# Optimization experiments

Hardware: AMD Instinct MI355X
Metric: run time of the kernel (lower is better)

## Reference

```python
import jax, jax.numpy as jnp
import numpy as np

N_NODES = 50000
N_EDGES = 800000
HIDDEN = 128


def setup_inputs() -> dict:
    key = jax.random.key(0)
    k_emb, k_ei, k1, k2, k3, kb1, kb2, kb3 = jax.random.split(key, 8)
    emb = jax.random.normal(k_emb, (N_NODES, HIDDEN), dtype=jnp.float32)
    edge_index = jax.random.randint(k_ei, (2, N_EDGES), 0, N_NODES, dtype=jnp.int64)
    h = HIDDEN
    # MLP([2h, 4h, h, 1]) weights, Kaiming-uniform-ish init
    def lin(k, fan_in, fan_out):
        bound = 1.0 / np.sqrt(fan_in)
        return jax.random.uniform(k, (fan_in, fan_out), jnp.float32, -bound, bound)
    W1 = lin(k1, 2 * h, 4 * h)
    b1 = jax.random.uniform(kb1, (4 * h,), jnp.float32, -1.0 / np.sqrt(2 * h), 1.0 / np.sqrt(2 * h))
    W2 = lin(k2, 4 * h, h)
    b2 = jax.random.uniform(kb2, (h,), jnp.float32, -1.0 / np.sqrt(4 * h), 1.0 / np.sqrt(4 * h))
    W3 = lin(k3, h, 1)
    b3 = jax.random.uniform(kb3, (1,), jnp.float32, -1.0 / np.sqrt(h), 1.0 / np.sqrt(h))
    return {"emb": emb, "edge_index": edge_index,
            "W1": W1, "b1": b1, "W2": W2, "b2": b2, "W3": W3, "b3": b3}


def reference(emb, edge_index, W1, b1, W2, b2, W3, b3):
    # learn_edge_att=True path: gather endpoints, concat, 3-layer MLP
    col, row = edge_index[0], edge_index[1]
    f12 = jnp.concatenate([emb[col], emb[row]], axis=-1)  # [E, 2h]
    x = jax.nn.relu(f12 @ W1 + b1)                         # [E, 4h]
    x = jax.nn.relu(x @ W2 + b2)                           # [E, h]
    att_log_logits = x @ W3 + b3                           # [E, 1]
    return att_log_logits
```

## Files before the change

### kernel.cpp

```cpp
#include <hip/hip_runtime.h>
#include <hip/hip_bf16.h>
#include <stdint.h>

#define N_EDGES   800000
#define N_NODESC  50000
#define HID       128

typedef __attribute__((ext_vector_type(8))) short bf16x8;
typedef __attribute__((ext_vector_type(4))) float f32x4;
typedef __attribute__((ext_vector_type(4))) unsigned int u32x4;

__device__ __forceinline__ short f2bf(float f) {
    union { float f; uint32_t u; } v; v.f = f;
    uint32_t r = v.u + 0x7FFFu + ((v.u >> 16) & 1u);
    return (short)(r >> 16);
}

__device__ __forceinline__ uint32_t packbf2(float lo, float hi) {
    float2 t; t.x = lo; t.y = hi;
    __hip_bfloat162 h = __float22bfloat162_rn(t);
    uint32_t u;
    __builtin_memcpy(&u, &h, 4);
    return u;
}

__device__ __forceinline__ uint32_t addrelu2(uint32_t a, uint32_t b) {
    __hip_bfloat162 ha, hb;
    __builtin_memcpy(&ha, &a, 4);
    __builtin_memcpy(&hb, &b, 4);
    __hip_bfloat162 s = __hadd2(ha, hb);
    uint32_t x;
    __builtin_memcpy(&x, &s, 4);
    uint32_t neg = (x & 0x80008000u) >> 15;
    return x & ~(neg * 0xFFFFu);
}
__device__ __forceinline__ bf16x8 addrelu8(u32x4 p, u32x4 q) {
    u32x4 r;
    #pragma unroll
    for (int j = 0; j < 4; ++j) r[j] = addrelu2(p[j], q[j]);
    bf16x8 out;
    __builtin_memcpy(&out, &r, 16);
    return out;
}

#define PQ_OFF    0UL
#define W1S_OFF   102400000UL
#define W2S_OFF   (W1S_OFF + 262144UL)
#define CNT_OFF   (W2S_OFF + 131072UL)
#define BSUM_OFF  (CNT_OFF + 1605632UL)
#define SPK_OFF   (BSUM_OFF + 8192UL)
#define POS_OFF   (SPK_OFF + 3200000UL)
#define TMP_OFF   (POS_OFF + 3200000UL)

#define NBINS     50176
#define NSEG      8
#define SCAN_N    (NSEG * NBINS)
#define SCANA_BLOCKS 1568

__global__ __launch_bounds__(256) void swizzle_kernel(const float* __restrict__ W1,
                                                      const float* __restrict__ W2,
                                                      short* __restrict__ W1s,
                                                      short* __restrict__ W2s) {
    int t = blockIdx.x * 256 + threadIdx.x;
    int lane = t & 63;
    int kq = lane >> 4;
    int nn = lane & 15;
    if (t < 16384) {
        int frag = t >> 6;
        int kc = frag >> 6;
        int nt = frag & 63;
        int n = nt * 16 + nn;
        int kbase = kc * 32 + kq * 8;
        bf16x8 v;
        #pragma unroll
        for (int j = 0; j < 8; ++j) {
            int k = kbase + j;
            float f = (n < 512) ? W1[k * 512 + n] : W1[(128 + k) * 512 + (n - 512)];
            v[j] = f2bf(f);
        }
        *(bf16x8*)(W1s + frag * 512 + lane * 8) = v;
    } else if (t < 24576) {
        int t2 = t - 16384;
        int frag = t2 >> 6;
        int kc = frag >> 3;
        int nt = frag & 7;
        int n = nt * 16 + nn;
        int kbase = kc * 32 + kq * 8;
        bf16x8 v;
        #pragma unroll
        for (int j = 0; j < 8; ++j) v[j] = f2bf(W2[(kbase + j) * HID + n]);
        *(bf16x8*)(W2s + frag * 512 + lane * 8) = v;
    }
}

__global__ __launch_bounds__(256) void precompute_kernel(const float* __restrict__ emb,
                                                         const short* __restrict__ W1s,
                                                         const float* __restrict__ b1,
                                                         short* __restrict__ PQ) {
    __shared__ short tile[4][16][272];
    int lane = threadIdx.x & 63;
    int w = threadIdx.x >> 6;
    int nb = blockIdx.x * 16;
    int m = lane & 15;
    int kq = lane >> 4;

    const float* arow = emb + (size_t)(nb + m) * 128 + kq * 8;

    f32x4 acc[16];
    #pragma unroll
    for (int i = 0; i < 16; ++i) acc[i] = (f32x4){0.f, 0.f, 0.f, 0.f};

    #pragma unroll
    for (int kc = 0; kc < 4; ++kc) {
        f32x4 x0 = *(const f32x4*)(arow + kc * 32);
        f32x4 x1 = *(const f32x4*)(arow + kc * 32 + 4);
        u32x4 au;
        au[0] = packbf2(x0[0], x0[1]); au[1] = packbf2(x0[2], x0[3]);
        au[2] = packbf2(x1[0], x1[1]); au[3] = packbf2(x1[2], x1[3]);
        bf16x8 a;
        __builtin_memcpy(&a, &au, 16);
        #pragma unroll
        for (int nt = 0; nt < 16; ++nt) {
            int frag = kc * 64 + (w * 16 + nt);
            bf16x8 b = *(const bf16x8*)(W1s + frag * 512 + lane * 8);
            acc[nt] = __builtin_amdgcn_mfma_f32_16x16x32_bf16(a, b, acc[nt], 0, 0, 0);
        }
    }

    #pragma unroll
    for (int nt = 0; nt < 16; ++nt) {
        int n = w * 256 + nt * 16 + m;
        float bias = (n < 512) ? b1[n] : 0.0f;
        #pragma unroll
        for (int r = 0; r < 4; ++r)
            tile[w][kq * 4 + r][nt * 16 + m] = f2bf(acc[nt][r] + bias);
    }

    #pragma unroll
    for (int s = 0; s < 8; ++s) {
        int row = s * 2 + (lane >> 5);
        int chunk = lane & 31;
        bf16x8 v = *(const bf16x8*)(&tile[w][row][chunk * 8]);
        *(bf16x8*)(PQ + (size_t)(nb + row) * 1024 + w * 256 + chunk * 8) = v;
    }
}


__global__ __launch_bounds__(256) void hist_kernel(const int* __restrict__ ei,
                                                   int* __restrict__ counts) {
    int e = blockIdx.x * 256 + threadIdx.x;
    int seg = blockIdx.x & 7;
    atomicAdd(&counts[seg * NBINS + ei[e]], 1);
}

__global__ __launch_bounds__(256) void scanA_kernel(int* __restrict__ counts,
                                                    int* __restrict__ bsum) {
    __shared__ int sm[256];
    int t = threadIdx.x;
    int e = blockIdx.x * 256 + t;
    int addr = (e & 7) * NBINS + (e >> 3);
    int v = counts[addr];
    sm[t] = v;
    __syncthreads();
    #pragma unroll
    for (int off = 1; off < 256; off <<= 1) {
        int y = (t >= off) ? sm[t - off] : 0;
        __syncthreads();
        sm[t] += y;
        __syncthreads();
    }
    counts[addr] = sm[t] - v;
    if (t == 255) bsum[blockIdx.x] = sm[t];
}

__global__ __launch_bounds__(256) void finalizeC_kernel(int* __restrict__ counts,
                                                        const int* __restrict__ bsum) {
    __shared__ int wsum[4];
    int t = threadIdx.x;
    int b = blockIdx.x;
    int v = 0;
    for (int idx = t; idx < b; idx += 256) v += bsum[idx];
    #pragma unroll
    for (int off = 1; off < 64; off <<= 1) v += __shfl_xor(v, off, 64);
    if ((t & 63) == 0) wsum[t >> 6] = v;
    __syncthreads();
    int base = wsum[0] + wsum[1] + wsum[2] + wsum[3];
    int e = b * 256 + t;
    counts[(e & 7) * NBINS + (e >> 3)] += base;
}

__global__ __launch_bounds__(256) void scatter_kernel(const int* __restrict__ ei,
                                                      int* __restrict__ cursor,
                                                      unsigned int* __restrict__ spk,
                                                      int* __restrict__ pos) {
    int e = blockIdx.x * 256 + threadIdx.x;
    int seg = blockIdx.x & 7;
    int c = ei[e];
    int r = ei[N_EDGES + e];
    int p = atomicAdd(&cursor[seg * NBINS + c], 1);
    spk[p] = ((unsigned int)r << 16) | (unsigned int)c;
    pos[e] = p;
}

__global__ __launch_bounds__(256, 3) void edge_kernel(const short* __restrict__ PQ,
                                                      const unsigned int* __restrict__ spk,
                                                      const short* __restrict__ W2s,
                                                      const float* __restrict__ b2,
                                                      const float* __restrict__ W3,
                                                      const float* __restrict__ b3,
                                                      float* __restrict__ tmp) {
    int lane = threadIdx.x & 63;
    int w = threadIdx.x >> 6;
    int e0 = blockIdx.x * 128 + w * 32;
    int m = lane & 15;
    int kq = lane >> 4;

    unsigned int pk = spk[e0 + (lane & 31)];

    const short* pb[2];
    const short* qb[2];
    #pragma unroll
    for (int t = 0; t < 2; ++t) {
        unsigned int v = __shfl(pk, t * 16 + m, 64);
        int ce = (int)(v & 0xFFFFu);
        int re = (int)(v >> 16);
        pb[t] = PQ + (size_t)ce * 1024 + kq * 8;
        qb[t] = PQ + (size_t)re * 1024 + 512 + kq * 8;
    }

    f32x4 acc[2][8];
    #pragma unroll
    for (int t = 0; t < 2; ++t)
        #pragma unroll
        for (int nt = 0; nt < 8; ++nt) acc[t][nt] = (f32x4){0.f, 0.f, 0.f, 0.f};

    #pragma unroll
    for (int kc = 0; kc < 16; ++kc) {
        u32x4 p[2], q[2];
        #pragma unroll
        for (int t = 0; t < 2; ++t) {
            p[t] = *(const u32x4*)(pb[t] + kc * 32);
            q[t] = *(const u32x4*)(qb[t] + kc * 32);
        }
        bf16x8 b[8];
        #pragma unroll
        for (int nt = 0; nt < 8; ++nt)
            b[nt] = *(const bf16x8*)(W2s + (kc * 8 + nt) * 512 + lane * 8);
        #pragma unroll
        for (int t = 0; t < 2; ++t) {
            bf16x8 a = addrelu8(p[t], q[t]);
            #pragma unroll
            for (int nt = 0; nt < 8; ++nt)
                acc[t][nt] = __builtin_amdgcn_mfma_f32_16x16x32_bf16(a, b[nt], acc[t][nt], 0, 0, 0);
        }
    }

    float b2v[8], w3v[8];
    #pragma unroll
    for (int nt = 0; nt < 8; ++nt) {
        b2v[nt] = b2[nt * 16 + m];
        w3v[nt] = W3[nt * 16 + m];
    }
    float b3s = b3[0];
    #pragma unroll
    for (int t = 0; t < 2; ++t) {
        float partial[4] = {0.f, 0.f, 0.f, 0.f};
        #pragma unroll
        for (int nt = 0; nt < 8; ++nt) {
            #pragma unroll
            for (int r = 0; r < 4; ++r) {
                float x2 = acc[t][nt][r] + b2v[nt];
                x2 = x2 > 0.f ? x2 : 0.f;
                partial[r] += x2 * w3v[nt];
            }
        }
        #pragma unroll
        for (int r = 0; r < 4; ++r) {
            #pragma unroll
            for (int off = 1; off < 16; off <<= 1)
                partial[r] += __shfl_xor(partial[r], off, 64);
        }
        if (m == 0) {
            f32x4 v;
            #pragma unroll
            for (int r = 0; r < 4; ++r) v[r] = partial[r] + b3s;
            *(f32x4*)(tmp + e0 + t * 16 + kq * 4) = v;
        }
    }
}

__global__ __launch_bounds__(256) void permute_kernel(const float* __restrict__ tmp,
                                                      const int* __restrict__ pos,
                                                      float* __restrict__ out) {
    int e = blockIdx.x * 256 + threadIdx.x;
    out[e] = tmp[pos[e]];
}

extern "C" void kernel_launch(void* const* d_in, const int* in_sizes, int n_in,
                              void* d_out, int out_size, void* d_ws, size_t ws_size,
                              hipStream_t stream) {
    const float* emb = (const float*)d_in[0];
    const int*   ei  = (const int*)d_in[1];
    const float* W1  = (const float*)d_in[2];
    const float* b1  = (const float*)d_in[3];
    const float* W2  = (const float*)d_in[4];
    const float* b2  = (const float*)d_in[5];
    const float* W3  = (const float*)d_in[6];
    const float* b3  = (const float*)d_in[7];
    float* out = (float*)d_out;

    short* PQ   = (short*)((char*)d_ws + PQ_OFF);
    short* W1s  = (short*)((char*)d_ws + W1S_OFF);
    short* W2s  = (short*)((char*)d_ws + W2S_OFF);
    int* counts = (int*)((char*)d_ws + CNT_OFF);
    int* bsum   = (int*)((char*)d_ws + BSUM_OFF);
    unsigned int* spk = (unsigned int*)((char*)d_ws + SPK_OFF);
    int* pos    = (int*)((char*)d_ws + POS_OFF);
    float* tmp  = (float*)((char*)d_ws + TMP_OFF);

    swizzle_kernel<<<96, 256, 0, stream>>>(W1, W2, W1s, W2s);
    hipMemsetAsync(counts, 0, SCAN_N * sizeof(int), stream);
    hist_kernel<<<N_EDGES / 256, 256, 0, stream>>>(ei, counts);
    scanA_kernel<<<SCANA_BLOCKS, 256, 0, stream>>>(counts, bsum);
    finalizeC_kernel<<<SCANA_BLOCKS, 256, 0, stream>>>(counts, bsum);
    scatter_kernel<<<N_EDGES / 256, 256, 0, stream>>>(ei, counts, spk, pos);

    precompute_kernel<<<N_NODESC / 16, 256, 0, stream>>>(emb, W1s, b1, PQ);
    edge_kernel<<<N_EDGES / 128, 256, 0, stream>>>(PQ, spk, W2s, b2, W3, b3, tmp);
    permute_kernel<<<N_EDGES / 256, 256, 0, stream>>>(tmp, pos, out);
}
```

Measured before the change: 452.9 us.

## Replace global-atomic counting sort with coarse-bin per-block LDS histogram sort

Swaps the exact per-node counting sort (global atomics over 8 segmented copies of 50k bins) for a coarse 16-node-bin sort built from per-block LDS histograms over 128 blocks, followed by the same scan and a per-block LDS cursor scatter. This removes the memset and the global atomic traffic in the histogram and scatter phases. Edges end up only partially sorted (grouped by col>>4), which may weaken gather locality in edge_kernel. Using only 128 blocks for the histogram and scatter may also underfill the GPU.

```diff
diff --git a/kernel.cpp b/kernel.cpp
--- a/kernel.cpp
+++ b/kernel.cpp
@@ -52,10 +52,11 @@
 #define POS_OFF   (SPK_OFF + 3200000UL)
 #define TMP_OFF   (POS_OFF + 3200000UL)
 
-#define NBINS     50176
-#define NSEG      8
-#define SCAN_N    (NSEG * NBINS)
-#define SCANA_BLOCKS 1568
+#define NBIN2     3136
+#define NBLK2     128
+#define EPB       (N_EDGES / NBLK2)
+#define SCAN_N    (NBIN2 * NBLK2)
+#define SCAN_BLOCKS 1568
 
 __global__ __launch_bounds__(256) void swizzle_kernel(const float* __restrict__ W1,
                                                       const float* __restrict__ W2,
@@ -146,20 +147,27 @@
 }
 
 
-__global__ __launch_bounds__(256) void hist_kernel(const int* __restrict__ ei,
-                                                   int* __restrict__ counts) {
-    int e = blockIdx.x * 256 + threadIdx.x;
-    int seg = blockIdx.x & 7;
-    atomicAdd(&counts[seg * NBINS + ei[e]], 1);
-}
-
-__global__ __launch_bounds__(256) void scanA_kernel(int* __restrict__ counts,
+__global__ __launch_bounds__(256) void binhist_kernel(const int* __restrict__ ei,
+                                                      int* __restrict__ cnt) {
+    __shared__ int h[NBIN2];
+    int t = threadIdx.x;
+    int b = blockIdx.x;
+    for (int i = t; i < NBIN2; i += 256) h[i] = 0;
+    __syncthreads();
+    int base = b * EPB;
+    for (int i = t; i < EPB; i += 256)
+        atomicAdd(&h[ei[base + i] >> 4], 1);
+    __syncthreads();
+    for (int i = t; i < NBIN2; i += 256) cnt[b * NBIN2 + i] = h[i];
+}
+
+__global__ __launch_bounds__(256) void scanA_kernel(int* __restrict__ cnt,
                                                     int* __restrict__ bsum) {
     __shared__ int sm[256];
     int t = threadIdx.x;
-    int e = blockIdx.x * 256 + t;
-    int addr = (e & 7) * NBINS + (e >> 3);
-    int v = counts[addr];
+    int L = blockIdx.x * 256 + t;
+    int addr = (L & (NBLK2 - 1)) * NBIN2 + (L >> 7);
+    int v = cnt[addr];
     sm[t] = v;
     __syncthreads();
     #pragma unroll
@@ -169,11 +177,11 @@
         sm[t] += y;
         __syncthreads();
     }
-    counts[addr] = sm[t] - v;
+    cnt[addr] = sm[t] - v;
     if (t == 255) bsum[blockIdx.x] = sm[t];
 }
 
-__global__ __launch_bounds__(256) void finalizeC_kernel(int* __restrict__ counts,
+__global__ __launch_bounds__(256) void finalizeC_kernel(int* __restrict__ cnt,
                                                         const int* __restrict__ bsum) {
     __shared__ int wsum[4];
     int t = threadIdx.x;
@@ -185,21 +193,28 @@
     if ((t & 63) == 0) wsum[t >> 6] = v;
     __syncthreads();
     int base = wsum[0] + wsum[1] + wsum[2] + wsum[3];
-    int e = b * 256 + t;
-    counts[(e & 7) * NBINS + (e >> 3)] += base;
-}
-
-__global__ __launch_bounds__(256) void scatter_kernel(const int* __restrict__ ei,
-                                                      int* __restrict__ cursor,
-                                                      unsigned int* __restrict__ spk,
-                                                      int* __restrict__ pos) {
-    int e = blockIdx.x * 256 + threadIdx.x;
-    int seg = blockIdx.x & 7;
-    int c = ei[e];
-    int r = ei[N_EDGES + e];
-    int p = atomicAdd(&cursor[seg * NBINS + c], 1);
-    spk[p] = ((unsigned int)r << 16) | (unsigned int)c;
-    pos[e] = p;
+    int L = b * 256 + t;
+    cnt[(L & (NBLK2 - 1)) * NBIN2 + (L >> 7)] += base;
+}
+
+__global__ __launch_bounds__(256) void binscatter_kernel(const int* __restrict__ ei,
+                                                         const int* __restrict__ cnt,
+                                                         unsigned int* __restrict__ spk,
+                                                         int* __restrict__ pos) {
+    __shared__ int cur[NBIN2];
+    int t = threadIdx.x;
+    int b = blockIdx.x;
+    for (int i = t; i < NBIN2; i += 256) cur[i] = cnt[b * NBIN2 + i];
+    __syncthreads();
+    int base = b * EPB;
+    for (int i = t; i < EPB; i += 256) {
+        int e = base + i;
+        int c = ei[e];
+        int r = ei[N_EDGES + e];
+        int p = atomicAdd(&cur[c >> 4], 1);
+        spk[p] = ((unsigned int)r << 16) | (unsigned int)c;
+        pos[e] = p;
+    }
 }
 
 __global__ __launch_bounds__(256, 3) void edge_kernel(const short* __restrict__ PQ,
@@ -312,18 +327,17 @@
     short* PQ   = (short*)((char*)d_ws + PQ_OFF);
     short* W1s  = (short*)((char*)d_ws + W1S_OFF);
     short* W2s  = (short*)((char*)d_ws + W2S_OFF);
-    int* counts = (int*)((char*)d_ws + CNT_OFF);
+    int* cnt    = (int*)((char*)d_ws + CNT_OFF);
     int* bsum   = (int*)((char*)d_ws + BSUM_OFF);
     unsigned int* spk = (unsigned int*)((char*)d_ws + SPK_OFF);
     int* pos    = (int*)((char*)d_ws + POS_OFF);
     float* tmp  = (float*)((char*)d_ws + TMP_OFF);
 
     swizzle_kernel<<<96, 256, 0, stream>>>(W1, W2, W1s, W2s);
-    hipMemsetAsync(counts, 0, SCAN_N * sizeof(int), stream);
-    hist_kernel<<<N_EDGES / 256, 256, 0, stream>>>(ei, counts);
-    scanA_kernel<<<SCANA_BLOCKS, 256, 0, stream>>>(counts, bsum);
-    finalizeC_kernel<<<SCANA_BLOCKS, 256, 0, stream>>>(counts, bsum);
-    scatter_kernel<<<N_EDGES / 256, 256, 0, stream>>>(ei, counts, spk, pos);
+    binhist_kernel<<<NBLK2, 256, 0, stream>>>(ei, cnt);
+    scanA_kernel<<<SCAN_BLOCKS, 256, 0, stream>>>(cnt, bsum);
+    finalizeC_kernel<<<SCAN_BLOCKS, 256, 0, stream>>>(cnt, bsum);
+    binscatter_kernel<<<NBLK2, 256, 0, stream>>>(ei, cnt, spk, pos);
 
     precompute_kernel<<<N_NODESC / 16, 256, 0, stream>>>(emb, W1s, b1, PQ);
     edge_kernel<<<N_EDGES / 128, 256, 0, stream>>>(PQ, spk, W2s, b2, W3, b3, tmp);
```

Measured after the change: 449.4 us. Within noise of the previous version (-0.8%).
